# Kernel tuning notes

Measured on AMD Instinct MI355X. Metric: run time of the kernel, lower is better.

Reference implementation:

```python
import jax, jax.numpy as jnp
import numpy as np
from jax.scipy.special import erf

Z = 87
NREF = 7
NC = 5
NW = 23
N_ATOMS = 75000
N_PAIRS = 1500000
BOHR = 0.5291772105638411
HARTREE = 27.211386024367243
K4, K5, K6, KK = 4.10451, 19.08857, 254.5553148552, 7.5
E3 = float(np.exp(3.0))

def _sp_inv(x):
    # inverse of softplus, so that softplus(raw) == x
    return float(np.log(np.expm1(x)))

def compute_refc6(scale_q_raw, refsys, zeff, refh, sscale, secaiw, gam, ascale, alphaiw, hcount, cpw):
    # gather per-reference-system atomic data via refsys indices [Z, NREF]
    zeff_r = zeff[refsys][..., None]
    sscale_r = sscale[refsys][..., None]
    secaiw_r = secaiw[refsys]            # [Z, NREF, NW]
    gam_r = gam[refsys][..., None]
    refh_i = refh[..., None] * jax.nn.softplus(scale_q_raw)[0]
    qmod = zeff_r + refh_i
    qsafe = jnp.where(qmod > 1e-8, qmod, 1.0)
    zfac = jnp.where(qmod > 1e-8, jnp.exp(3.0 * (1.0 - jnp.exp(2.0 * gam_r * (1.0 - zeff_r / qsafe)))), E3)
    alpha = sscale_r * secaiw_r * zfac
    alpha = jnp.maximum(ascale[..., None] * (alphaiw - hcount[..., None] * alpha), 0.0)  # [Z, NREF, NW]
    # Casimir-Polder integration: refc6[i,j,a,b] = 3/(2pi) * sum_w alpha[i,a,w]*alpha[j,b,w]*w
    return (3.0 / (2.0 * np.pi)) * jnp.einsum('iaw,jbw,w->ijab', alpha, alpha, cpw)

def _forward(species, edge_index, lengths, partial_charges, s6_raw, s8_raw, a1_raw, a2_raw, scale_q_raw, refsys, zeff, refh, sscale, secaiw, gam, ascale, alphaiw, hcount, cpw, rcov, en, ncount_mask, ncount_weight, cn, fixgweights, refq, sqrt_r4r2):
    n = species.shape[0]
    idx_i, idx_j = edge_index[0], edge_index[1]
    r = lengths * (1.0 / BOHR)
    sp_i, sp_j = species[idx_i], species[idx_j]
    # erf-based coordination number
    rcov_ij = (4.0 / 3.0) * (rcov[sp_i] + rcov[sp_j])
    den = K4 * jnp.exp(-((jnp.abs(en[sp_i] - en[sp_j]) + K5) ** 2) / K6)
    countf = den * 0.5 * (1.0 + erf(-KK * (r - rcov_ij) / rcov_ij))
    ncoord = jax.ops.segment_sum(countf, idx_i, num_segments=n)  # [N]
    # Gaussian reference weights over (NREF, NC)
    nce = ncoord[:, None, None]
    gw = jnp.exp(-6.0 * ncount_weight[species] * (nce - cn[species]) ** 2)
    gw = jnp.sum(ncount_mask[species] * gw, axis=-1)  # [N, NREF]
    norm = jnp.clip(jnp.sum(gw, axis=-1, keepdims=True), 1e-7, None)
    gw = jnp.where(norm > 1e-8, gw / norm, fixgweights[species])
    # charge scaling zeta
    spq = jax.nn.softplus(scale_q_raw)[0]
    zeff_s = zeff[species][:, None]
    qref = zeff_s + refq[species] * spq
    qmod = zeff_s + partial_charges[:, None]
    qsafe = jnp.where(qmod > 1e-8, qmod, 1.0)
    zeta = jnp.where(qmod > 1e-8, jnp.exp(3.0 * (1.0 - jnp.exp(2.0 * gam[species][:, None] * (1.0 - qref / qsafe)))), E3) * gw  # [N, NREF]
    # pairwise C6 via reference C6 table
    refc6 = compute_refc6(scale_q_raw, refsys, zeff, refh, sscale, secaiw, gam, ascale, alphaiw, hcount, cpw)
    c6 = jnp.einsum('pab,pa,pb->p', refc6[sp_i, sp_j], zeta[idx_i], zeta[idx_j])  # [P]
    # Becke-Johnson damped -C6/r^6 - C8/r^8
    r4r2 = 3.0 * sqrt_r4r2[sp_i] * sqrt_r4r2[sp_j]
    a1 = jax.nn.softplus(a1_raw)[0]
    a2 = jax.nn.softplus(a2_raw)[0]
    s6 = jax.nn.softplus(s6_raw)[0]
    s8 = jax.nn.softplus(s8_raw)[0]
    r0sq = (a1 * jnp.sqrt(r4r2) + a2) ** 2
    r2 = r * r
    r6 = r2 * r2 * r2
    r8 = r6 * r2
    pair = -c6 * (s6 / (r6 + r0sq ** 3) + s8 * r4r2 / (r8 + r0sq ** 4))
    # per-atom dispersion energy in eV (0.5 because each pair counted twice in edge list)
    return 0.5 * HARTREE * jax.ops.segment_sum(pair, idx_i, num_segments=n)

def setup_inputs():
    key = jax.random.key(0)
    ks = jax.random.split(key, 24)
    u = lambda k, sh, lo, hi: jax.random.uniform(k, sh, jnp.float32, lo, hi)
    return {
        'species': jax.random.randint(ks[0], (N_ATOMS,), 0, Z),
        'edge_index': jax.random.randint(ks[1], (2, N_PAIRS), 0, N_ATOMS),
        'lengths': u(ks[2], (N_PAIRS,), 1.5, 6.0),
        'partial_charges': 0.1 * jax.random.normal(ks[3], (N_ATOMS,), jnp.float32),
        's6_raw': jnp.array([_sp_inv(1.0)], jnp.float32),
        's8_raw': jnp.array([_sp_inv(1.61679827)], jnp.float32),
        'a1_raw': jnp.array([_sp_inv(0.44959224)], jnp.float32),
        'a2_raw': jnp.array([_sp_inv(3.35743605)], jnp.float32),
        'scale_q_raw': jnp.array([_sp_inv(1.0)], jnp.float32),
        'refsys': jax.random.randint(ks[4], (Z, NREF), 0, Z),
        'zeff': u(ks[5], (Z,), 1.0, 10.0),
        'refh': u(ks[6], (Z, NREF), -0.5, 0.5),
        'sscale': u(ks[7], (Z,), 0.5, 1.5),
        'secaiw': u(ks[8], (Z, NW), 0.1, 5.0),
        'gam': u(ks[9], (Z,), 0.1, 0.5),
        'ascale': u(ks[10], (Z, NREF), 0.5, 1.5),
        'alphaiw': u(ks[11], (Z, NREF, NW), 0.5, 20.0),
        'hcount': u(ks[12], (Z, NREF), 0.0, 3.0),
        'cpw': u(ks[13], (NW,), 0.01, 0.5),
        'rcov': u(ks[14], (Z,), 0.5, 3.0),
        'en': u(ks[15], (Z,), 0.8, 4.0),
        'ncount_mask': (jax.random.uniform(ks[16], (Z, NREF, NC)) > 0.5).astype(jnp.float32),
        'ncount_weight': u(ks[17], (Z, NREF, NC), 0.5, 2.0),
        'cn': u(ks[18], (Z, NREF, NC), 0.0, 6.0),
        'fixgweights': jnp.full((Z, NREF), 1.0 / NREF, jnp.float32),
        'refq': u(ks[19], (Z, NREF), -0.5, 0.5),
        'sqrt_r4r2': u(ks[20], (Z,), 2.0, 10.0),
    }

def reference(species, edge_index, lengths, partial_charges, s6_raw, s8_raw, a1_raw, a2_raw, scale_q_raw, refsys, zeff, refh, sscale, secaiw, gam, ascale, alphaiw, hcount, cpw, rcov, en, ncount_mask, ncount_weight, cn, fixgweights, refq, sqrt_r4r2):
    return _forward(species, edge_index, lengths, partial_charges, s6_raw, s8_raw, a1_raw, a2_raw, scale_q_raw, refsys, zeff, refh, sscale, secaiw, gam, ascale, alphaiw, hcount, cpw, rcov, en, ncount_mask, ncount_weight, cn, fixgweights, refq, sqrt_r4r2)
```

## Files before the change

### kernel.cpp

```cpp
#include <hip/hip_runtime.h>
#include <hip/hip_bf16.h>
#include <hip/hip_fp16.h>

#define ZZ      87
#define NREF    7
#define NC      5
#define NW      23
#define NATOMS  75000
#define NPAIRS  1500000
#define IAW     (ZZ*NREF*NW)

#define BSH     7
#define BSZ     128
#define NB      586
#define BLKP    2048
#define NBLK    733

#define OFF_ALPHA   32
#define OFF_AD      14040
#define OFF_NCOORD  164040
#define OFF_ENERGY  239040
#define OFF_BETA    314048
#define OFF_HIST    1214048
#define OFF_LIMG    OFF_HIST
#define OFF_BTOT    1643586
#define OFF_BBASE   1644176
#define OFF_REC     1644768
#define SORT_WS_NEED      ((size_t)(OFF_REC + 2*NPAIRS) * 4)

#define IMG_A   0
#define IMG_C   7308
#define IMG_Q   13398
#define IMG_G   14008
#define IMG_DW  14356

static constexpr float INV_BOHR  = (float)(1.0/0.5291772105638411);
static constexpr float HALF_HART = (float)(0.5*27.211386024367243);
static constexpr float CK4 = 4.10451f;
static constexpr float CK5 = 19.08857f;
static constexpr float INV_K6 = (float)(1.0/254.5553148552);
static constexpr float CKK = 7.5f;
static constexpr float E3F = 20.085536923187668f;
static constexpr float C32PI = 0.47746482927568606f;

__device__ __forceinline__ bool detect_bf16(const void* s6raw) {
    return ((*(const unsigned short*)s6raw) >> 8) == 0x3Fu;
}
__device__ __forceinline__ float ldf(const void* p, int i, bool bf) {
    if (bf) {
        unsigned int u = ((const unsigned short*)p)[i];
        return __uint_as_float(u << 16);
    }
    return ((const float*)p)[i];
}
__device__ __forceinline__ float splus(float x) {
    return (x > 15.f) ? x : log1pf(expf(x));
}
__device__ __forceinline__ void up2(unsigned int u, float* d) {
    __half2 h;
    *reinterpret_cast<unsigned int*>(&h) = u;
    float2 f = __half22float2(h);
    d[0] = f.x; d[1] = f.y;
}
__device__ __forceinline__ void unpack24(uint4 a, uint4 b, uint4 c, float* v) {
    up2(a.x, v+0);  up2(a.y, v+2);  up2(a.z, v+4);  up2(a.w, v+6);
    up2(b.x, v+8);  up2(b.y, v+10); up2(b.z, v+12); up2(b.w, v+14);
    up2(c.x, v+16); up2(c.y, v+18); up2(c.z, v+20); up2(c.w, v+22);
}
__device__ __forceinline__ void ld8(const void* p, int p0, bool bf, float* L) {
    if (bf) {
        uint4 u = *(const uint4*)((const unsigned short*)p + p0);
        unsigned vs[4] = {u.x, u.y, u.z, u.w};
        #pragma unroll
        for (int k = 0; k < 4; ++k) {
            L[2*k]   = __uint_as_float(vs[k] << 16);
            L[2*k+1] = __uint_as_float(vs[k] & 0xFFFF0000u);
        }
    } else {
        float4 f0 = *(const float4*)((const float*)p + p0);
        float4 f1 = *(const float4*)((const float*)p + p0 + 4);
        L[0]=f0.x; L[1]=f0.y; L[2]=f0.z; L[3]=f0.w;
        L[4]=f1.x; L[5]=f1.y; L[6]=f1.z; L[7]=f1.w;
    }
}

__global__ void k_prep(const int* __restrict__ refsys, const int* __restrict__ species,
                       const void* zeff, const void* refh, const void* sscale,
                       const void* secaiw, const void* gam, const void* ascale,
                       const void* alphaiw, const void* hcount, const void* cpw,
                       const void* rcov, const void* en,
                       const void* s6r, const void* s8r, const void* a1r,
                       const void* a2r, const void* sqr,
                       float* __restrict__ ws) {
    const bool bf = detect_bf16(s6r);
    int t = blockIdx.x * blockDim.x + threadIdx.x;
    if (t == 0) {
        ws[0] = splus(ldf(sqr, 0, bf));
        ws[1] = splus(ldf(s6r, 0, bf));
        ws[2] = splus(ldf(s8r, 0, bf));
        ws[3] = splus(ldf(a1r, 0, bf));
        ws[4] = splus(ldf(a2r, 0, bf));
    }
    if (t < NATOMS) {
        int sp = species[t];
        ((float2*)(ws + OFF_AD))[t] = make_float2(ldf(rcov, sp, bf), ldf(en, sp, bf));
    }
    if (t >= IAW) return;

    int w  = t % NW;
    int ia = t / NW;
    int rs = refsys[ia];
    float spq  = splus(ldf(sqr, 0, bf));
    float ze   = ldf(zeff, rs, bf);
    float qmod = ze + ldf(refh, ia, bf) * spq;
    float zfac;
    if (qmod > 1e-8f) {
        float g = ldf(gam, rs, bf);
        zfac = expf(3.f * (1.f - expf(2.f * g * (1.f - ze / qmod))));
    } else {
        zfac = E3F;
    }
    float sec = ldf(sscale, rs, bf) * ldf(secaiw, rs*NW + w, bf) * zfac;
    float al  = ldf(ascale, ia, bf) *
                (ldf(alphaiw, ia*NW + w, bf) - ldf(hcount, ia, bf) * sec);
    float bsw = sqrtf(C32PI * ldf(cpw, w, bf));
    ws[OFF_ALPHA + t] = fmaxf(al, 0.f) * bsw;
}

__global__ void k_pack(const void* zeff, const void* gam, const void* mask,
                       const void* wght, const void* cn, const void* refq,
                       const void* sq4, const void* s6r,
                       float* __restrict__ ws) {
    const bool bf = detect_bf16(s6r);
    unsigned* img = (unsigned*)(ws + OFF_LIMG);
    int t = blockIdx.x * blockDim.x + threadIdx.x;
    if (t < 7308) {
        int row = t / 12, u = t % 12;
        int w0 = 2*u, w1 = 2*u + 1;
        const float* aF = ws + OFF_ALPHA + row * NW;
        float v0 = aF[w0];
        float v1 = (w1 < NW) ? aF[w1] : 0.f;
        unsigned lo = __half_as_ushort(__float2half(v0));
        unsigned hi = __half_as_ushort(__float2half(v1));
        img[t] = lo | (hi << 16);
    } else if (t < 7308 + 3045) {
        int e = t - 7308;
        float cnv = ldf(cn, e, bf);
        float wv  = (ldf(mask, e, bf) > 0.5f) ? ldf(wght, e, bf) : -1.f;
        ((float2*)(img + IMG_C))[e] = make_float2(cnv, wv);
    } else if (t < 10353 + 609) {
        int e = t - 10353;
        int sp = e / NREF;
        ((float*)(img + IMG_Q))[e] = ldf(zeff, sp, bf) + ldf(refq, e, bf) * ws[0];
    } else if (t < 10962 + 87) {
        int sp = t - 10962;
        ((float4*)(img + IMG_G))[sp] = make_float4(ldf(zeff, sp, bf),
                                                   ldf(gam, sp, bf),
                                                   ldf(sq4, sp, bf), 0.f);
    } else if (t == 11049) {
        img[14007] = 0;
    }
}


__global__ void k_hist(const int* __restrict__ eidx, int* __restrict__ hist) {
    __shared__ int h[NB];
    int blk = blockIdx.x;
    for (int t = threadIdx.x; t < NB; t += 256) h[t] = 0;
    __syncthreads();
    int p0 = blk * BLKP + (int)threadIdx.x * 8;
    if (p0 + 8 <= NPAIRS) {
        int4 a0 = *(const int4*)(eidx + p0);
        int4 a1 = *(const int4*)(eidx + p0 + 4);
        atomicAdd(&h[a0.x >> BSH], 1);
        atomicAdd(&h[a0.y >> BSH], 1);
        atomicAdd(&h[a0.z >> BSH], 1);
        atomicAdd(&h[a0.w >> BSH], 1);
        atomicAdd(&h[a1.x >> BSH], 1);
        atomicAdd(&h[a1.y >> BSH], 1);
        atomicAdd(&h[a1.z >> BSH], 1);
        atomicAdd(&h[a1.w >> BSH], 1);
    }
    __syncthreads();
    for (int t = threadIdx.x; t < NB; t += 256)
        hist[(size_t)blk * NB + t] = h[t];
}

__global__ __launch_bounds__(1024) void k_scan_bucket(int* __restrict__ hist,
                                                      int* __restrict__ btot) {
    int b = blockIdx.x;
    int t = threadIdx.x;
    int v = (t < NBLK) ? hist[(size_t)t * NB + b] : 0;
    int lane = t & 63, wid = t >> 6;
    int x = v;
    #pragma unroll
    for (int d = 1; d < 64; d <<= 1) {
        int n = __shfl_up(x, d, 64);
        if (lane >= d) x += n;
    }
    __shared__ int wsum[16];
    if (lane == 63) wsum[wid] = x;
    __syncthreads();
    if (t == 0) {
        int acc = 0;
        #pragma unroll
        for (int w = 0; w < 16; ++w) { int s = wsum[w]; wsum[w] = acc; acc += s; }
    }
    __syncthreads();
    int incl = x + wsum[wid];
    if (t < NBLK) hist[(size_t)t * NB + b] = incl - v;
    if (t == 1023) btot[b] = incl;
}

__global__ __launch_bounds__(1024) void k_scan_base(const int* __restrict__ btot,
                                                    int* __restrict__ bbase) {
    int t = threadIdx.x;
    int v = (t < NB) ? btot[t] : 0;
    int lane = t & 63, wid = t >> 6;
    int x = v;
    #pragma unroll
    for (int d = 1; d < 64; d <<= 1) {
        int n = __shfl_up(x, d, 64);
        if (lane >= d) x += n;
    }
    __shared__ int wsum[16];
    if (lane == 63) wsum[wid] = x;
    __syncthreads();
    if (t == 0) {
        int acc = 0;
        #pragma unroll
        for (int w = 0; w < 16; ++w) { int s = wsum[w]; wsum[w] = acc; acc += s; }
    }
    __syncthreads();
    int incl = x + wsum[wid];
    if (t < NB) bbase[t] = incl - v;
    if (t == 1023) bbase[NB] = incl;
}

__global__ void k_scatter(const int* __restrict__ eidx, const void* lengths,
                          const void* s6r, const int* __restrict__ hist,
                          const int* __restrict__ bbase, uint2* __restrict__ rec) {
    const bool bf = detect_bf16(s6r);
    __shared__ int cnt[NB];
    int blk = blockIdx.x;
    const int* hcol = hist + (size_t)blk * NB;
    for (int t = threadIdx.x; t < NB; t += 256)
        cnt[t] = bbase[t] + hcol[t];
    __syncthreads();
    int p0 = blk * BLKP + (int)threadIdx.x * 8;
    if (p0 + 8 > NPAIRS) return;
    int4 a0 = *(const int4*)(eidx + p0);
    int4 a1 = *(const int4*)(eidx + p0 + 4);
    int4 b0 = *(const int4*)(eidx + NPAIRS + p0);
    int4 b1 = *(const int4*)(eidx + NPAIRS + p0 + 4);
    float L[8];
    ld8(lengths, p0, bf, L);
    int is[8] = {a0.x,a0.y,a0.z,a0.w,a1.x,a1.y,a1.z,a1.w};
    int js[8] = {b0.x,b0.y,b0.z,b0.w,b1.x,b1.y,b1.z,b1.w};
    #pragma unroll
    for (int k = 0; k < 8; ++k) {
        int b = is[k] >> BSH;
        int pos = atomicAdd(&cnt[b], 1);
        rec[pos] = make_uint2(((unsigned)(is[k] & (BSZ-1)) << 17) | (unsigned)js[k],
                              __float_as_uint(L[k]));
    }
}

__global__ __launch_bounds__(512) void k_ncoord_s(const uint2* __restrict__ rec,
        const int* __restrict__ bbase, float* __restrict__ ws) {
    __shared__ float bins[BSZ];
    __shared__ float adl[BSZ * 2];
    int b = blockIdx.x;
    int a0 = b << BSH;
    int na = NATOMS - a0; if (na > BSZ) na = BSZ;
    for (int t = threadIdx.x; t < BSZ; t += 512) bins[t] = 0.f;
    const float2* AD = (const float2*)(ws + OFF_AD);
    for (int t = threadIdx.x; t < na; t += 512) {
        float2 v = AD[a0 + t];
        adl[2*t] = v.x; adl[2*t + 1] = v.y;
    }
    __syncthreads();
    int bs = bbase[b], be = bbase[b + 1];
    for (int p = bs + (int)threadIdx.x; p < be; p += 2*512) {
        int p2 = p + 512;
        bool h2 = (p2 < be);
        uint2 r1 = rec[p];
        uint2 r2 = h2 ? rec[p2] : r1;
        int il1 = (r1.x >> 17) & (BSZ-1), j1 = r1.x & 0x1FFFF;
        int il2 = (r2.x >> 17) & (BSZ-1), j2 = r2.x & 0x1FFFF;
        float2 aj1 = AD[j1];
        float2 aj2 = AD[j2];
        {
            float r  = __uint_as_float(r1.y) * INV_BOHR;
            float rc = (4.f/3.f) * (adl[2*il1] + aj1.x);
            float d  = fabsf(adl[2*il1+1] - aj1.y) + CK5;
            float cf = CK4 * expf(-(d*d)*INV_K6) * 0.5f * (1.f + erff(-CKK*(r-rc)/rc));
            atomicAdd(&bins[il1], cf);
        }
        if (h2) {
            float r  = __uint_as_float(r2.y) * INV_BOHR;
            float rc = (4.f/3.f) * (adl[2*il2] + aj2.x);
            float d  = fabsf(adl[2*il2+1] - aj2.y) + CK5;
            float cf = CK4 * expf(-(d*d)*INV_K6) * 0.5f * (1.f + erff(-CKK*(r-rc)/rc));
            atomicAdd(&bins[il2], cf);
        }
    }
    __syncthreads();
    for (int t = threadIdx.x; t < na; t += 512) ws[OFF_NCOORD + a0 + t] = bins[t];
}

__global__ __launch_bounds__(256) void k_beta(const int* __restrict__ species,
                       const void* pq, const void* s6r, float* __restrict__ ws) {
    const bool bf = detect_bf16(s6r);
    __shared__ __align__(16) unsigned s_img[IMG_DW];
    {
        const uint4* g4 = (const uint4*)(ws + OFF_LIMG);
        uint4* s4 = (uint4*)s_img;
        for (int t = threadIdx.x; t < IMG_DW/4; t += 256) s4[t] = g4[t];
    }
    __syncthreads();
    const unsigned* sA = s_img;
    const float2*   sC = (const float2*)(s_img + IMG_C);
    const float*    sQ = (const float*)(s_img + IMG_Q);
    const float4*   sG = (const float4*)(s_img + IMG_G);

    for (int k = blockIdx.x * 256 + threadIdx.x; k < NATOMS; k += 256 * 256) {
        int sp = species[k];
        float nce = ws[OFF_NCOORD + k];
        float4 zg = sG[sp];
        float qmod = zg.x + ldf(pq, k, bf);

        float gw[NREF];
        float sum = 0.f;
        #pragma unroll
        for (int a = 0; a < NREF; ++a) {
            float g = 0.f;
            #pragma unroll
            for (int c = 0; c < NC; ++c) {
                float2 cw = sC[sp*35 + a*NC + c];
                float dlt = nce - cw.x;
                float e = __expf(-6.f * cw.y * dlt * dlt);
                g += (cw.y > 0.f) ? e : 0.f;
            }
            gw[a] = g; sum += g;
        }
        float inv = 1.f / fmaxf(sum, 1e-7f);

        float2 acc[12];
        #pragma unroll
        for (int u = 0; u < 12; ++u) acc[u] = make_float2(0.f, 0.f);

        #pragma unroll
        for (int a = 0; a < NREF; ++a) {
            float qref = sQ[sp*NREF + a];
            float zf = (qmod > 1e-8f)
                     ? __expf(3.f * (1.f - __expf(2.f * zg.y * (1.f - qref / qmod))))
                     : E3F;
            float za = zf * gw[a] * inv;
            const uint2* ar = (const uint2*)(sA + (sp*NREF + a) * 12);
            #pragma unroll
            for (int u2 = 0; u2 < 6; ++u2) {
                uint2 h = ar[u2];
                float f[4];
                up2(h.x, f); up2(h.y, f+2);
                acc[2*u2].x   = fmaf(f[0], za, acc[2*u2].x);
                acc[2*u2].y   = fmaf(f[1], za, acc[2*u2].y);
                acc[2*u2+1].x = fmaf(f[2], za, acc[2*u2+1].x);
                acc[2*u2+1].y = fmaf(f[3], za, acc[2*u2+1].y);
            }
        }

        alignas(16) __half hrow[24];
        #pragma unroll
        for (int u = 0; u < 12; ++u) {
            hrow[2*u]   = __float2half(acc[u].x);
            hrow[2*u+1] = __float2half(acc[u].y);
        }
        hrow[23] = __float2half(zg.z);

        uint4* dst = (uint4*)((char*)(ws + OFF_BETA) + (size_t)k * 48);
        const uint4* src = (const uint4*)hrow;
        dst[0] = src[0]; dst[1] = src[1]; dst[2] = src[2];
    }
}

__device__ __forceinline__ float pair_energy(const float* vi, const float* vj,
                                             float len, float s6, float s8,
                                             float a1, float a2) {
    float c6 = 0.f;
    #pragma unroll
    for (int w = 0; w < NW; ++w) c6 = fmaf(vi[w], vj[w], c6);
    float rr = 3.f * vi[23] * vj[23];
    float r  = len * INV_BOHR;
    float r2 = r * r;
    float r6 = r2 * r2 * r2;
    float r8 = r6 * r2;
    float r0   = a1 * sqrtf(rr) + a2;
    float r0sq = r0 * r0;
    float r0_6 = r0sq * r0sq * r0sq;
    float r0_8 = r0_6 * r0sq;
    return -c6 * (s6 / (r6 + r0_6) + s8 * rr / (r8 + r0_8));
}

__global__ __launch_bounds__(512) void k_energy_s(const uint2* __restrict__ rec,
        const int* __restrict__ bbase, const float* __restrict__ ws,
        void* __restrict__ out, const void* s6r) {
    const bool bf = detect_bf16(s6r);
    __shared__ float bins[BSZ];
    __shared__ unsigned irow[BSZ * 13];
    int b = blockIdx.x;
    int a0 = b << BSH;
    int na = NATOMS - a0; if (na > BSZ) na = BSZ;
    for (int t = threadIdx.x; t < BSZ; t += 512) bins[t] = 0.f;
    const unsigned* betaU = (const unsigned*)(ws + OFF_BETA);
    for (int t = threadIdx.x; t < na * 12; t += 512) {
        int l = t / 12, k = t - l * 12;
        irow[l * 13 + k] = betaU[(size_t)(a0 + l) * 12 + k];
    }
    __syncthreads();
    float s6 = ws[1], s8 = ws[2], a1 = ws[3], a2 = ws[4];
    int bs = bbase[b], be = bbase[b + 1];
    const char* B = (const char*)betaU;
    for (int p = bs + (int)threadIdx.x; p < be; p += 2*512) {
        int p2 = p + 512;
        bool h2 = (p2 < be);
        uint2 r1 = rec[p];
        uint2 r2 = h2 ? rec[p2] : r1;
        int il1 = (r1.x >> 17) & (BSZ-1), j1 = r1.x & 0x1FFFF;
        int il2 = (r2.x >> 17) & (BSZ-1), j2 = r2.x & 0x1FFFF;
        const uint4* J1 = (const uint4*)(B + (size_t)j1 * 48);
        const uint4* J2 = (const uint4*)(B + (size_t)j2 * 48);
        uint4 ja0 = J1[0], ja1 = J1[1], ja2 = J1[2];
        uint4 jb0 = J2[0], jb1 = J2[1], jb2 = J2[2];
        float vi[24], vj[24];
        #pragma unroll
        for (int k = 0; k < 12; ++k) up2(irow[il1*13 + k], vi + 2*k);
        unpack24(ja0, ja1, ja2, vj);
        float e1 = pair_energy(vi, vj, __uint_as_float(r1.y), s6, s8, a1, a2);
        atomicAdd(&bins[il1], e1);
        if (h2) {
            #pragma unroll
            for (int k = 0; k < 12; ++k) up2(irow[il2*13 + k], vi + 2*k);
            unpack24(jb0, jb1, jb2, vj);
            float e2 = pair_energy(vi, vj, __uint_as_float(r2.y), s6, s8, a1, a2);
            atomicAdd(&bins[il2], e2);
        }
    }
    __syncthreads();
    for (int t = threadIdx.x; t < na; t += 512) {
        float v = HALF_HART * bins[t];
        if (bf) ((__hip_bfloat16*)out)[a0 + t] = __float2bfloat16(v);
        else    ((float*)out)[a0 + t] = v;
    }
}


__device__ __forceinline__ float2 ldf2(const void* p, int t, bool bf) {
    if (bf) {
        unsigned int u = ((const unsigned int*)p)[t];
        return make_float2(__uint_as_float(u << 16),
                           __uint_as_float(u & 0xFFFF0000u));
    }
    return ((const float2*)p)[t];
}

__global__ void k_ncoord_fb(const int* __restrict__ eidx, const void* lengths,
                            const void* s6r, float* __restrict__ ws) {
    const bool bf = detect_bf16(s6r);
    int t = blockIdx.x * blockDim.x + threadIdx.x;
    if (2*t >= NPAIRS) return;
    int2 ii = ((const int2*)eidx)[t];
    int2 jj = ((const int2*)(eidx + NPAIRS))[t];
    float2 L = ldf2(lengths, t, bf);
    const float2* AD = (const float2*)(ws + OFF_AD);
    float2 ai = AD[ii.x], aj = AD[jj.x];
    float2 bi = AD[ii.y], bj = AD[jj.y];
    float r0  = L.x * INV_BOHR;
    float rc0 = (4.f/3.f) * (ai.x + aj.x);
    float d0  = fabsf(ai.y - aj.y) + CK5;
    float cf0 = CK4 * expf(-(d0*d0) * INV_K6) * 0.5f * (1.f + erff(-CKK * (r0 - rc0) / rc0));
    float r1  = L.y * INV_BOHR;
    float rc1 = (4.f/3.f) * (bi.x + bj.x);
    float d1  = fabsf(bi.y - bj.y) + CK5;
    float cf1 = CK4 * expf(-(d1*d1) * INV_K6) * 0.5f * (1.f + erff(-CKK * (r1 - rc1) / rc1));
    atomicAdd(ws + OFF_NCOORD + ii.x, cf0);
    atomicAdd(ws + OFF_NCOORD + ii.y, cf1);
}

__global__ void k_beta_fb(const int* __restrict__ species, const void* pq,
                          const void* zeff, const void* gam,
                          const void* mask, const void* wght, const void* cn,
                          const void* refq, const void* sq4, const void* s6r,
                          float* __restrict__ ws) {
    const bool bf = detect_bf16(s6r);
    int k = blockIdx.x * blockDim.x + threadIdx.x;
    if (k >= NATOMS) return;
    int sp = species[k];
    float nce = ws[OFF_NCOORD + k];
    float spq = ws[0];
    float gw[NREF];
    float sum = 0.f;
    #pragma unroll
    for (int a = 0; a < NREF; ++a) {
        float g = 0.f;
        #pragma unroll
        for (int c = 0; c < NC; ++c) {
            int idx = (sp*NREF + a)*NC + c;
            float dlt = nce - ldf(cn, idx, bf);
            g += ldf(mask, idx, bf) * expf(-6.f * ldf(wght, idx, bf) * dlt * dlt);
        }
        gw[a] = g; sum += g;
    }
    float inv  = 1.f / fmaxf(sum, 1e-7f);
    float ze   = ldf(zeff, sp, bf);
    float qmod = ze + ldf(pq, k, bf);
    float gm   = ldf(gam, sp, bf);
    float beta[NW];
    #pragma unroll
    for (int w = 0; w < NW; ++w) beta[w] = 0.f;
    const float* A = ws + OFF_ALPHA + sp * (NREF*NW);
    #pragma unroll
    for (int a = 0; a < NREF; ++a) {
        float qref = ze + ldf(refq, sp*NREF + a, bf) * spq;
        float zf = (qmod > 1e-8f)
                 ? expf(3.f * (1.f - expf(2.f * gm * (1.f - qref / qmod))))
                 : E3F;
        float za = zf * gw[a] * inv;
        #pragma unroll
        for (int w = 0; w < NW; ++w) beta[w] = fmaf(A[a*NW + w], za, beta[w]);
    }
    alignas(16) __half hrow[24];
    #pragma unroll
    for (int w = 0; w < NW; ++w) hrow[w] = __float2half(beta[w]);
    hrow[23] = __float2half(ldf(sq4, sp, bf));
    uint4* dst = (uint4*)((char*)(ws + OFF_BETA) + (size_t)k * 48);
    const uint4* src = (const uint4*)hrow;
    dst[0] = src[0]; dst[1] = src[1]; dst[2] = src[2];
}

__global__ void k_energy_fb(const int* __restrict__ eidx, const void* lengths,
                            const void* s6r, float* __restrict__ ws) {
    const bool bf = detect_bf16(s6r);
    int t = blockIdx.x * blockDim.x + threadIdx.x;
    if (2*t >= NPAIRS) return;
    int2 ii = ((const int2*)eidx)[t];
    int2 jj = ((const int2*)(eidx + NPAIRS))[t];
    float2 L = ldf2(lengths, t, bf);
    const char* B = (const char*)(ws + OFF_BETA);
    const uint4* qi0 = (const uint4*)(B + (size_t)ii.x * 48);
    const uint4* qj0 = (const uint4*)(B + (size_t)jj.x * 48);
    const uint4* qi1 = (const uint4*)(B + (size_t)ii.y * 48);
    const uint4* qj1 = (const uint4*)(B + (size_t)jj.y * 48);
    uint4 ra0 = qi0[0], ra1 = qi0[1], ra2 = qi0[2];
    uint4 rb0 = qj0[0], rb1 = qj0[1], rb2 = qj0[2];
    uint4 rc0 = qi1[0], rc1 = qi1[1], rc2 = qi1[2];
    uint4 rd0 = qj1[0], rd1 = qj1[1], rd2 = qj1[2];
    float s6 = ws[1], s8 = ws[2], a1 = ws[3], a2 = ws[4];
    float vi[24], vj[24];
    unpack24(ra0, ra1, ra2, vi);
    unpack24(rb0, rb1, rb2, vj);
    float e0 = pair_energy(vi, vj, L.x, s6, s8, a1, a2);
    unpack24(rc0, rc1, rc2, vi);
    unpack24(rd0, rd1, rd2, vj);
    float e1 = pair_energy(vi, vj, L.y, s6, s8, a1, a2);
    atomicAdd(ws + OFF_ENERGY + ii.x, e0);
    atomicAdd(ws + OFF_ENERGY + ii.y, e1);
}

__global__ void k_final(const float* __restrict__ ws, void* out, const void* s6r) {
    const bool bf = detect_bf16(s6r);
    int k = blockIdx.x * blockDim.x + threadIdx.x;
    if (k >= NATOMS) return;
    float v = HALF_HART * ws[OFF_ENERGY + k];
    if (bf) ((__hip_bfloat16*)out)[k] = __float2bfloat16(v);
    else    ((float*)out)[k] = v;
}

extern "C" void kernel_launch(void* const* d_in, const int* in_sizes, int n_in,
                              void* d_out, int out_size, void* d_ws, size_t ws_size,
                              hipStream_t stream) {
    (void)in_sizes; (void)n_in; (void)out_size;

    const int*  species = (const int*)d_in[0];
    const int*  eidx    = (const int*)d_in[1];
    const void* lengths = d_in[2];
    const void* pq      = d_in[3];
    const void* s6r     = d_in[4];
    const void* s8r     = d_in[5];
    const void* a1r     = d_in[6];
    const void* a2r     = d_in[7];
    const void* sqr     = d_in[8];
    const int*  refsys  = (const int*)d_in[9];
    const void* zeff    = d_in[10];
    const void* refh    = d_in[11];
    const void* sscale  = d_in[12];
    const void* secaiw  = d_in[13];
    const void* gam     = d_in[14];
    const void* ascale  = d_in[15];
    const void* alphaiw = d_in[16];
    const void* hcount  = d_in[17];
    const void* cpw     = d_in[18];
    const void* rcov    = d_in[19];
    const void* en      = d_in[20];
    const void* mask    = d_in[21];
    const void* wght    = d_in[22];
    const void* cn      = d_in[23];
    const void* refq    = d_in[25];
    const void* sq4     = d_in[26];

    float* ws = (float*)d_ws;
    const bool use_sort = (ws_size >= SORT_WS_NEED);

    k_prep<<<(NATOMS + 255)/256, 256, 0, stream>>>(refsys, species, zeff, refh,
            sscale, secaiw, gam, ascale, alphaiw, hcount, cpw, rcov, en,
            s6r, s8r, a1r, a2r, sqr, ws);

    if (use_sort) {
        int*   hist  = (int*)(ws + OFF_HIST);
        int*   btot  = (int*)(ws + OFF_BTOT);
        int*   bbase = (int*)(ws + OFF_BBASE);
        uint2* rec   = (uint2*)(ws + OFF_REC);

        k_hist       <<<NBLK, 256,  0, stream>>>(eidx, hist);
        k_scan_bucket<<<NB,   1024, 0, stream>>>(hist, btot);
        k_scan_base  <<<1,    1024, 0, stream>>>(btot, bbase);
        k_scatter    <<<NBLK, 256,  0, stream>>>(eidx, lengths, s6r, hist, bbase, rec);
        k_pack       <<<44,   256,  0, stream>>>(zeff, gam, mask, wght, cn,
                                                 refq, sq4, s6r, ws);
        k_ncoord_s   <<<NB,   512,  0, stream>>>(rec, bbase, ws);
        k_beta       <<<256,  256,  0, stream>>>(species, pq, s6r, ws);
        k_energy_s   <<<NB,   512,  0, stream>>>(rec, bbase, ws, d_out, s6r);
    } else {
        hipMemsetAsync(ws + OFF_NCOORD, 0, (size_t)(2 * NATOMS) * sizeof(float), stream);
        k_ncoord_fb<<<(NPAIRS/2 + 255)/256, 256, 0, stream>>>(eidx, lengths, s6r, ws);
        k_beta_fb  <<<(NATOMS   + 255)/256, 256, 0, stream>>>(species, pq, zeff, gam,
                        mask, wght, cn, refq, sq4, s6r, ws);
        k_energy_fb<<<(NPAIRS/2 + 255)/256, 256, 0, stream>>>(eidx, lengths, s6r, ws);
        k_final    <<<(NATOMS   + 255)/256, 256, 0, stream>>>(ws, d_out, s6r);
    }
}
```

Baseline: 87.34 us.

## Fuse prep into histogram, pack into scatter, and beta into ncoord kernels

```diff
diff --git a/kernel.cpp b/kernel.cpp
--- a/kernel.cpp
+++ b/kernel.cpp
@@ -13,16 +13,18 @@
 #define BSH     7
 #define BSZ     128
 #define NB      586
-#define BLKP    2048
-#define NBLK    733
+#define BLKP    4096
+#define NBLK    367
+#define PREP_BLKS 147
+#define PACK_BLKS 22
 
 #define OFF_ALPHA   32
 #define OFF_AD      14040
 #define OFF_NCOORD  164040
 #define OFF_ENERGY  239040
+#define OFF_IMG     OFF_ENERGY
 #define OFF_BETA    314048
 #define OFF_HIST    1214048
-#define OFF_LIMG    OFF_HIST
 #define OFF_BTOT    1643586
 #define OFF_BBASE   1644176
 #define OFF_REC     1644768
@@ -84,16 +86,14 @@
     }
 }
 
-__global__ void k_prep(const int* __restrict__ refsys, const int* __restrict__ species,
-                       const void* zeff, const void* refh, const void* sscale,
-                       const void* secaiw, const void* gam, const void* ascale,
-                       const void* alphaiw, const void* hcount, const void* cpw,
-                       const void* rcov, const void* en,
-                       const void* s6r, const void* s8r, const void* a1r,
-                       const void* a2r, const void* sqr,
-                       float* __restrict__ ws) {
-    const bool bf = detect_bf16(s6r);
-    int t = blockIdx.x * blockDim.x + threadIdx.x;
+__device__ __forceinline__ void prep_body(int t, bool bf,
+        const int* __restrict__ refsys, const int* __restrict__ species,
+        const void* zeff, const void* refh, const void* sscale,
+        const void* secaiw, const void* gam, const void* ascale,
+        const void* alphaiw, const void* hcount, const void* cpw,
+        const void* rcov, const void* en,
+        const void* s6r, const void* s8r, const void* a1r,
+        const void* a2r, const void* sqr, float* __restrict__ ws) {
     if (t == 0) {
         ws[0] = splus(ldf(sqr, 0, bf));
         ws[1] = splus(ldf(s6r, 0, bf));
@@ -106,7 +106,6 @@
         ((float2*)(ws + OFF_AD))[t] = make_float2(ldf(rcov, sp, bf), ldf(en, sp, bf));
     }
     if (t >= IAW) return;
-
     int w  = t % NW;
     int ia = t / NW;
     int rs = refsys[ia];
@@ -127,48 +126,30 @@
     ws[OFF_ALPHA + t] = fmaxf(al, 0.f) * bsw;
 }
 
-__global__ void k_pack(const void* zeff, const void* gam, const void* mask,
-                       const void* wght, const void* cn, const void* refq,
-                       const void* sq4, const void* s6r,
-                       float* __restrict__ ws) {
-    const bool bf = detect_bf16(s6r);
-    unsigned* img = (unsigned*)(ws + OFF_LIMG);
-    int t = blockIdx.x * blockDim.x + threadIdx.x;
-    if (t < 7308) {
-        int row = t / 12, u = t % 12;
-        int w0 = 2*u, w1 = 2*u + 1;
-        const float* aF = ws + OFF_ALPHA + row * NW;
-        float v0 = aF[w0];
-        float v1 = (w1 < NW) ? aF[w1] : 0.f;
-        unsigned lo = __half_as_ushort(__float2half(v0));
-        unsigned hi = __half_as_ushort(__float2half(v1));
-        img[t] = lo | (hi << 16);
-    } else if (t < 7308 + 3045) {
-        int e = t - 7308;
-        float cnv = ldf(cn, e, bf);
-        float wv  = (ldf(mask, e, bf) > 0.5f) ? ldf(wght, e, bf) : -1.f;
-        ((float2*)(img + IMG_C))[e] = make_float2(cnv, wv);
-    } else if (t < 10353 + 609) {
-        int e = t - 10353;
-        int sp = e / NREF;
-        ((float*)(img + IMG_Q))[e] = ldf(zeff, sp, bf) + ldf(refq, e, bf) * ws[0];
-    } else if (t < 10962 + 87) {
-        int sp = t - 10962;
-        ((float4*)(img + IMG_G))[sp] = make_float4(ldf(zeff, sp, bf),
-                                                   ldf(gam, sp, bf),
-                                                   ldf(sq4, sp, bf), 0.f);
-    } else if (t == 11049) {
-        img[14007] = 0;
-    }
-}
-
-
-__global__ void k_hist(const int* __restrict__ eidx, int* __restrict__ hist) {
+
+__global__ __launch_bounds__(512) void k_prep_hist(
+        const int* __restrict__ refsys, const int* __restrict__ species,
+        const void* zeff, const void* refh, const void* sscale,
+        const void* secaiw, const void* gam, const void* ascale,
+        const void* alphaiw, const void* hcount, const void* cpw,
+        const void* rcov, const void* en,
+        const void* s6r, const void* s8r, const void* a1r,
+        const void* a2r, const void* sqr,
+        const int* __restrict__ eidx, int* __restrict__ hist,
+        float* __restrict__ ws) {
+    const bool bf = detect_bf16(s6r);
     __shared__ int h[NB];
     int blk = blockIdx.x;
-    for (int t = threadIdx.x; t < NB; t += 256) h[t] = 0;
-    __syncthreads();
-    int p0 = blk * BLKP + (int)threadIdx.x * 8;
+    if (blk < PREP_BLKS) {
+        prep_body(blk * 512 + (int)threadIdx.x, bf, refsys, species, zeff, refh,
+                  sscale, secaiw, gam, ascale, alphaiw, hcount, cpw, rcov, en,
+                  s6r, s8r, a1r, a2r, sqr, ws);
+        return;
+    }
+    int hb = blk - PREP_BLKS;
+    for (int t = threadIdx.x; t < NB; t += 512) h[t] = 0;
+    __syncthreads();
+    int p0 = hb * BLKP + (int)threadIdx.x * 8;
     if (p0 + 8 <= NPAIRS) {
         int4 a0 = *(const int4*)(eidx + p0);
         int4 a1 = *(const int4*)(eidx + p0 + 4);
@@ -182,8 +163,8 @@
         atomicAdd(&h[a1.w >> BSH], 1);
     }
     __syncthreads();
-    for (int t = threadIdx.x; t < NB; t += 256)
-        hist[(size_t)blk * NB + t] = h[t];
+    for (int t = threadIdx.x; t < NB; t += 512)
+        hist[(size_t)hb * NB + t] = h[t];
 }
 
 __global__ __launch_bounds__(1024) void k_scan_bucket(int* __restrict__ hist,
@@ -237,14 +218,49 @@
     if (t == 1023) bbase[NB] = incl;
 }
 
-__global__ void k_scatter(const int* __restrict__ eidx, const void* lengths,
-                          const void* s6r, const int* __restrict__ hist,
-                          const int* __restrict__ bbase, uint2* __restrict__ rec) {
+__global__ __launch_bounds__(512) void k_scatter_pack(
+        const int* __restrict__ eidx, const void* lengths, const void* s6r,
+        const int* __restrict__ hist, const int* __restrict__ bbase,
+        uint2* __restrict__ rec,
+        const void* zeff, const void* gam, const void* mask,
+        const void* wght, const void* cn, const void* refq, const void* sq4,
+        float* __restrict__ ws) {
     const bool bf = detect_bf16(s6r);
     __shared__ int cnt[NB];
     int blk = blockIdx.x;
+    if (blk >= NBLK) {
+        unsigned* img = (unsigned*)(ws + OFF_IMG);
+        int t = (blk - NBLK) * 512 + (int)threadIdx.x;
+        if (t < 7308) {
+            int row = t / 12, u = t % 12;
+            int w0 = 2*u, w1 = 2*u + 1;
+            const float* aF = ws + OFF_ALPHA + row * NW;
+            float v0 = aF[w0];
+            float v1 = (w1 < NW) ? aF[w1] : 0.f;
+            unsigned lo = __half_as_ushort(__float2half(v0));
+            unsigned hi = __half_as_ushort(__float2half(v1));
+            img[t] = lo | (hi << 16);
+        } else if (t < 7308 + 3045) {
+            int e = t - 7308;
+            float cnv = ldf(cn, e, bf);
+            float wv  = (ldf(mask, e, bf) > 0.5f) ? ldf(wght, e, bf) : -1.f;
+            ((float2*)(img + IMG_C))[e] = make_float2(cnv, wv);
+        } else if (t < 10353 + 609) {
+            int e = t - 10353;
+            int sp = e / NREF;
+            ((float*)(img + IMG_Q))[e] = ldf(zeff, sp, bf) + ldf(refq, e, bf) * ws[0];
+        } else if (t < 10962 + 87) {
+            int sp = t - 10962;
+            ((float4*)(img + IMG_G))[sp] = make_float4(ldf(zeff, sp, bf),
+                                                       ldf(gam, sp, bf),
+                                                       ldf(sq4, sp, bf), 0.f);
+        } else if (t == 11049) {
+            img[14007] = 0;
+        }
+        return;
+    }
     const int* hcol = hist + (size_t)blk * NB;
-    for (int t = threadIdx.x; t < NB; t += 256)
+    for (int t = threadIdx.x; t < NB; t += 512)
         cnt[t] = bbase[t] + hcol[t];
     __syncthreads();
     int p0 = blk * BLKP + (int)threadIdx.x * 8;
@@ -266,13 +282,21 @@
     }
 }
 
-__global__ __launch_bounds__(512) void k_ncoord_s(const uint2* __restrict__ rec,
-        const int* __restrict__ bbase, float* __restrict__ ws) {
+__global__ __launch_bounds__(512) void k_ncbeta(const uint2* __restrict__ rec,
+        const int* __restrict__ bbase, const int* __restrict__ species,
+        const void* pq, const void* s6r, float* __restrict__ ws) {
+    const bool bf = detect_bf16(s6r);
+    __shared__ __align__(16) unsigned s_img[IMG_DW];
     __shared__ float bins[BSZ];
     __shared__ float adl[BSZ * 2];
     int b = blockIdx.x;
     int a0 = b << BSH;
     int na = NATOMS - a0; if (na > BSZ) na = BSZ;
+    {
+        const uint4* g4 = (const uint4*)(ws + OFF_IMG);
+        uint4* s4 = (uint4*)s_img;
+        for (int t = threadIdx.x; t < IMG_DW/4; t += 512) s4[t] = g4[t];
+    }
     for (int t = threadIdx.x; t < BSZ; t += 512) bins[t] = 0.f;
     const float2* AD = (const float2*)(ws + OFF_AD);
     for (int t = threadIdx.x; t < na; t += 512) {
@@ -306,82 +330,67 @@
         }
     }
     __syncthreads();
-    for (int t = threadIdx.x; t < na; t += 512) ws[OFF_NCOORD + a0 + t] = bins[t];
-}
-
-__global__ __launch_bounds__(256) void k_beta(const int* __restrict__ species,
-                       const void* pq, const void* s6r, float* __restrict__ ws) {
-    const bool bf = detect_bf16(s6r);
-    __shared__ __align__(16) unsigned s_img[IMG_DW];
-    {
-        const uint4* g4 = (const uint4*)(ws + OFF_LIMG);
-        uint4* s4 = (uint4*)s_img;
-        for (int t = threadIdx.x; t < IMG_DW/4; t += 256) s4[t] = g4[t];
-    }
-    __syncthreads();
+    int t = threadIdx.x;
+    if (t >= na) return;
+    int k = a0 + t;
     const unsigned* sA = s_img;
     const float2*   sC = (const float2*)(s_img + IMG_C);
     const float*    sQ = (const float*)(s_img + IMG_Q);
     const float4*   sG = (const float4*)(s_img + IMG_G);
 
-    for (int k = blockIdx.x * 256 + threadIdx.x; k < NATOMS; k += 256 * 256) {
-        int sp = species[k];
-        float nce = ws[OFF_NCOORD + k];
-        float4 zg = sG[sp];
-        float qmod = zg.x + ldf(pq, k, bf);
-
-        float gw[NREF];
-        float sum = 0.f;
-        #pragma unroll
-        for (int a = 0; a < NREF; ++a) {
-            float g = 0.f;
-            #pragma unroll
-            for (int c = 0; c < NC; ++c) {
-                float2 cw = sC[sp*35 + a*NC + c];
-                float dlt = nce - cw.x;
-                float e = __expf(-6.f * cw.y * dlt * dlt);
-                g += (cw.y > 0.f) ? e : 0.f;
-            }
-            gw[a] = g; sum += g;
-        }
-        float inv = 1.f / fmaxf(sum, 1e-7f);
-
-        float2 acc[12];
-        #pragma unroll
-        for (int u = 0; u < 12; ++u) acc[u] = make_float2(0.f, 0.f);
-
-        #pragma unroll
-        for (int a = 0; a < NREF; ++a) {
-            float qref = sQ[sp*NREF + a];
-            float zf = (qmod > 1e-8f)
-                     ? __expf(3.f * (1.f - __expf(2.f * zg.y * (1.f - qref / qmod))))
-                     : E3F;
-            float za = zf * gw[a] * inv;
-            const uint2* ar = (const uint2*)(sA + (sp*NREF + a) * 12);
-            #pragma unroll
-            for (int u2 = 0; u2 < 6; ++u2) {
-                uint2 h = ar[u2];
-                float f[4];
-                up2(h.x, f); up2(h.y, f+2);
-                acc[2*u2].x   = fmaf(f[0], za, acc[2*u2].x);
-                acc[2*u2].y   = fmaf(f[1], za, acc[2*u2].y);
-                acc[2*u2+1].x = fmaf(f[2], za, acc[2*u2+1].x);
-                acc[2*u2+1].y = fmaf(f[3], za, acc[2*u2+1].y);
-            }
-        }
-
-        alignas(16) __half hrow[24];
-        #pragma unroll
-        for (int u = 0; u < 12; ++u) {
-            hrow[2*u]   = __float2half(acc[u].x);
-            hrow[2*u+1] = __float2half(acc[u].y);
-        }
-        hrow[23] = __float2half(zg.z);
-
-        uint4* dst = (uint4*)((char*)(ws + OFF_BETA) + (size_t)k * 48);
-        const uint4* src = (const uint4*)hrow;
-        dst[0] = src[0]; dst[1] = src[1]; dst[2] = src[2];
-    }
+    int sp = species[k];
+    float nce = bins[t];
+    float4 zg = sG[sp];
+    float qmod = zg.x + ldf(pq, k, bf);
+
+    float gw[NREF];
+    float sum = 0.f;
+    #pragma unroll
+    for (int a = 0; a < NREF; ++a) {
+        float g = 0.f;
+        #pragma unroll
+        for (int c = 0; c < NC; ++c) {
+            float2 cw = sC[sp*35 + a*NC + c];
+            float dlt = nce - cw.x;
+            float e = __expf(-6.f * cw.y * dlt * dlt);
+            g += (cw.y > 0.f) ? e : 0.f;
+        }
+        gw[a] = g; sum += g;
+    }
+    float inv = 1.f / fmaxf(sum, 1e-7f);
+
+    float2 acc[12];
+    #pragma unroll
+    for (int u = 0; u < 12; ++u) acc[u] = make_float2(0.f, 0.f);
+    #pragma unroll
+    for (int a = 0; a < NREF; ++a) {
+        float qref = sQ[sp*NREF + a];
+        float zf = (qmod > 1e-8f)
+                 ? __expf(3.f * (1.f - __expf(2.f * zg.y * (1.f - qref / qmod))))
+                 : E3F;
+        float za = zf * gw[a] * inv;
+        const uint2* ar = (const uint2*)(sA + (sp*NREF + a) * 12);
+        #pragma unroll
+        for (int u2 = 0; u2 < 6; ++u2) {
+            uint2 h = ar[u2];
+            float f[4];
+            up2(h.x, f); up2(h.y, f+2);
+            acc[2*u2].x   = fmaf(f[0], za, acc[2*u2].x);
+            acc[2*u2].y   = fmaf(f[1], za, acc[2*u2].y);
+            acc[2*u2+1].x = fmaf(f[2], za, acc[2*u2+1].x);
+            acc[2*u2+1].y = fmaf(f[3], za, acc[2*u2+1].y);
+        }
+    }
+    alignas(16) __half hrow[24];
+    #pragma unroll
+    for (int u = 0; u < 12; ++u) {
+        hrow[2*u]   = __float2half(acc[u].x);
+        hrow[2*u+1] = __float2half(acc[u].y);
+    }
+    hrow[23] = __float2half(zg.z);
+    uint4* dst = (uint4*)((char*)(ws + OFF_BETA) + (size_t)k * 48);
+    const uint4* src = (const uint4*)hrow;
+    dst[0] = src[0]; dst[1] = src[1]; dst[2] = src[2];
 }
 
 __device__ __forceinline__ float pair_energy(const float* vi, const float* vj,
@@ -454,6 +463,20 @@
     }
 }
 
+
+__global__ void k_prep_fb(const int* __restrict__ refsys, const int* __restrict__ species,
+                          const void* zeff, const void* refh, const void* sscale,
+                          const void* secaiw, const void* gam, const void* ascale,
+                          const void* alphaiw, const void* hcount, const void* cpw,
+                          const void* rcov, const void* en,
+                          const void* s6r, const void* s8r, const void* a1r,
+                          const void* a2r, const void* sqr,
+                          float* __restrict__ ws) {
+    const bool bf = detect_bf16(s6r);
+    prep_body(blockIdx.x * blockDim.x + threadIdx.x, bf, refsys, species, zeff,
+              refh, sscale, secaiw, gam, ascale, alphaiw, hcount, cpw, rcov, en,
+              s6r, s8r, a1r, a2r, sqr, ws);
+}
 
 __device__ __forceinline__ float2 ldf2(const void* p, int t, bool bf) {
     if (bf) {
@@ -611,27 +634,28 @@
     float* ws = (float*)d_ws;
     const bool use_sort = (ws_size >= SORT_WS_NEED);
 
-    k_prep<<<(NATOMS + 255)/256, 256, 0, stream>>>(refsys, species, zeff, refh,
-            sscale, secaiw, gam, ascale, alphaiw, hcount, cpw, rcov, en,
-            s6r, s8r, a1r, a2r, sqr, ws);
-
     if (use_sort) {
         int*   hist  = (int*)(ws + OFF_HIST);
         int*   btot  = (int*)(ws + OFF_BTOT);
         int*   bbase = (int*)(ws + OFF_BBASE);
         uint2* rec   = (uint2*)(ws + OFF_REC);
 
-        k_hist       <<<NBLK, 256,  0, stream>>>(eidx, hist);
-        k_scan_bucket<<<NB,   1024, 0, stream>>>(hist, btot);
-        k_scan_base  <<<1,    1024, 0, stream>>>(btot, bbase);
-        k_scatter    <<<NBLK, 256,  0, stream>>>(eidx, lengths, s6r, hist, bbase, rec);
-        k_pack       <<<44,   256,  0, stream>>>(zeff, gam, mask, wght, cn,
-                                                 refq, sq4, s6r, ws);
-        k_ncoord_s   <<<NB,   512,  0, stream>>>(rec, bbase, ws);
-        k_beta       <<<256,  256,  0, stream>>>(species, pq, s6r, ws);
-        k_energy_s   <<<NB,   512,  0, stream>>>(rec, bbase, ws, d_out, s6r);
+        k_prep_hist  <<<PREP_BLKS + NBLK, 512, 0, stream>>>(refsys, species,
+                         zeff, refh, sscale, secaiw, gam, ascale, alphaiw,
+                         hcount, cpw, rcov, en, s6r, s8r, a1r, a2r, sqr,
+                         eidx, hist, ws);
+        k_scan_bucket<<<NB, 1024, 0, stream>>>(hist, btot);
+        k_scan_base  <<<1,  1024, 0, stream>>>(btot, bbase);
+        k_scatter_pack<<<NBLK + PACK_BLKS, 512, 0, stream>>>(eidx, lengths, s6r,
+                         hist, bbase, rec, zeff, gam, mask, wght, cn, refq,
+                         sq4, ws);
+        k_ncbeta     <<<NB, 512, 0, stream>>>(rec, bbase, species, pq, s6r, ws);
+        k_energy_s   <<<NB, 512, 0, stream>>>(rec, bbase, ws, d_out, s6r);
     } else {
         hipMemsetAsync(ws + OFF_NCOORD, 0, (size_t)(2 * NATOMS) * sizeof(float), stream);
+        k_prep_fb  <<<(NATOMS   + 511)/512, 512, 0, stream>>>(refsys, species,
+                        zeff, refh, sscale, secaiw, gam, ascale, alphaiw,
+                        hcount, cpw, rcov, en, s6r, s8r, a1r, a2r, sqr, ws);
         k_ncoord_fb<<<(NPAIRS/2 + 255)/256, 256, 0, stream>>>(eidx, lengths, s6r, ws);
         k_beta_fb  <<<(NATOMS   + 255)/256, 256, 0, stream>>>(species, pq, zeff, gam,
                         mask, wght, cn, refq, sq4, s6r, ws);
```

Result: faster. 75.38 us (-13.7%).
